# Optimization experiments

Measured on AMD Instinct MI355X. Metric: run time of the kernel, lower is better.

Reference implementation:

```python
import jax, jax.numpy as jnp
import numpy as np


def setup_inputs() -> dict:
    key = jax.random.key(0)
    ks = jax.random.split(key, 6)
    T, B, I, H = 2048, 64, 512, 512
    return {
        "x_seq": jax.random.normal(ks[0], (T, B, I), dtype=jnp.float32),
        "h0": jax.random.normal(ks[1], (B, H), dtype=jnp.float32),
        "Wx_f": jax.random.normal(ks[2], (H, I), dtype=jnp.float32) * (1.0 / np.sqrt(I)),
        "Wh_f": jax.random.normal(ks[3], (H, H), dtype=jnp.float32) * (1.0 / np.sqrt(H)),
        "b_f": jnp.zeros((H,), dtype=jnp.float32),
        "Wx_h": jax.random.normal(ks[4], (H, I), dtype=jnp.float32) * (1.0 / np.sqrt(I)),
        "Wh_h": jax.random.normal(ks[5], (H, H), dtype=jnp.float32) * (1.0 / np.sqrt(H)),
        "b_h": jnp.zeros((H,), dtype=jnp.float32),
    }


def reference(x_seq, h0, Wx_f, Wh_f, b_f, Wx_h, Wh_h, b_h):
    # Precompute the input projections for all timesteps in two big GEMMs
    # (same math as per-step mm(x, Wx.T) + b inside the loop).
    xf = jnp.einsum("tbi,hi->tbh", x_seq, Wx_f) + b_f  # [T,B,H]
    xh = jnp.einsum("tbi,hi->tbh", x_seq, Wx_h) + b_h  # [T,B,H]

    def step(h, xs):
        xf_t, xh_t = xs
        f = jax.nn.sigmoid(xf_t + h @ Wh_f.T)           # forget gate [B,H]
        h_t = jnp.tanh((f * h) @ Wh_h.T + xh_t)          # candidate [B,H]
        h_new = (1.0 - f) * h + f * h_t                  # blend
        return h_new, h_new

    h_final, y_seq = jax.lax.scan(step, h0, (xf, xh))
    return y_seq, h_final
```

## Files before the change

kernel.cpp:

```cpp
#include <hip/hip_runtime.h>
#include <hip/hip_bf16.h>

#define T_STEPS 2048
#define BATCH   64
#define HID     512
#define NBG 2
#define NCG 16
#define CHUNK 32

typedef unsigned short u16;
typedef unsigned int u32;
typedef unsigned long long u64;
typedef __attribute__((ext_vector_type(4))) float f32x4;
typedef __attribute__((ext_vector_type(8))) short bf16x8;

static __device__ __forceinline__ u16 f2bf(float f) {
  union { float f; unsigned u; } v; v.f = f;
  unsigned u = v.u;
  return (u16)((u + 0x7fffu + ((u >> 16) & 1u)) >> 16);
}
static __device__ __forceinline__ float bf2f(u16 h) {
  union { unsigned u; float f; } v; v.u = ((unsigned)h) << 16; return v.f;
}

static __device__ __forceinline__ void st_rlx32(u32* p, u32 v) {
  __hip_atomic_store(p, v, __ATOMIC_RELAXED, __HIP_MEMORY_SCOPE_AGENT);
}
static __device__ __forceinline__ u64 ld_rlx64(const u64* p) {
  return __hip_atomic_load(p, __ATOMIC_RELAXED, __HIP_MEMORY_SCOPE_AGENT);
}
static __device__ __forceinline__ int ld_rlx_i(const int* p) {
  return __hip_atomic_load(p, __ATOMIC_RELAXED, __HIP_MEMORY_SCOPE_AGENT);
}
static __device__ __forceinline__ void st_rlx_i(int* p, int v) {
  __hip_atomic_store(p, v, __ATOMIC_RELAXED, __HIP_MEMORY_SCOPE_AGENT);
}

__global__ __launch_bounds__(256) void cvt_weights(
    const float* __restrict__ wxf, const float* __restrict__ wxh,
    const float* __restrict__ whf, const float* __restrict__ whh,
    u16* __restrict__ o_wxf, u16* __restrict__ o_wxh,
    u16* __restrict__ o_whf, u16* __restrict__ o_whh) {
  int i = blockIdx.x * 256 + threadIdx.x;
  o_wxf[i] = f2bf(wxf[i]);
  o_wxh[i] = f2bf(wxh[i]);
  o_whf[i] = f2bf(whf[i]);
  o_whh[i] = f2bf(whh[i]);
}

__global__ __launch_bounds__(256) void proj_gemm(
    const float* __restrict__ x,
    const u16* __restrict__ wxf, const u16* __restrict__ wxh,
    const float* __restrict__ b_f, const float* __restrict__ b_h,
    u16* __restrict__ xfo, u16* __restrict__ xho) {
  const int bid = blockIdx.x;
  const int mbase = (bid >> 4) * 64;
  const int nbase = (bid & 15) * 64;
  const int tid = threadIdx.x;
  const int lane = tid & 63, wv = tid >> 6;
  const int l15 = lane & 15, lhi = lane >> 4;
  __shared__ u16 a_lds[64 * 48];

  const u16* bptr[4];
#pragma unroll
  for (int ntt = 0; ntt < 4; ++ntt) {
    int n = nbase + ntt * 16 + l15;
    bptr[ntt] = (n < 512) ? (wxf + (size_t)n * 512) : (wxh + (size_t)(n - 512) * 512);
  }
  const int arow = tid >> 2;
  const int akq = (tid & 3) * 8;
  const float* asrc = x + (size_t)(mbase + arow) * 512 + akq;

  f32x4 acc[4];
#pragma unroll
  for (int i = 0; i < 4; ++i) acc[i] = (f32x4){0.f, 0.f, 0.f, 0.f};

  for (int kk = 0; kk < 512; kk += 32) {
    float4 v0 = *(const float4*)(asrc + kk);
    float4 v1 = *(const float4*)(asrc + kk + 4);
    u16* dst = &a_lds[arow * 48 + akq];
    dst[0] = f2bf(v0.x); dst[1] = f2bf(v0.y); dst[2] = f2bf(v0.z); dst[3] = f2bf(v0.w);
    dst[4] = f2bf(v1.x); dst[5] = f2bf(v1.y); dst[6] = f2bf(v1.z); dst[7] = f2bf(v1.w);
    __syncthreads();
    bf16x8 a = *(const bf16x8*)&a_lds[(wv * 16 + l15) * 48 + lhi * 8];
#pragma unroll
    for (int ntt = 0; ntt < 4; ++ntt) {
      bf16x8 b = *(const bf16x8*)(bptr[ntt] + kk + lhi * 8);
      acc[ntt] = __builtin_amdgcn_mfma_f32_16x16x32_bf16(a, b, acc[ntt], 0, 0, 0);
    }
    __syncthreads();
  }
#pragma unroll
  for (int ntt = 0; ntt < 4; ++ntt) {
    int n = nbase + ntt * 16 + l15;
    float bias = (n < 512) ? b_f[n] : b_h[n - 512];
    u16* op = (n < 512) ? (xfo + n) : (xho + (n - 512));
#pragma unroll
    for (int q = 0; q < 4; ++q) {
      int row = mbase + wv * 16 + lhi * 4 + q;
      op[(size_t)row * 512] = f2bf(acc[ntt][q] + bias);
    }
  }
}

__global__ __launch_bounds__(256) void mgu_scan(
    const float* __restrict__ h0,
    const u16* __restrict__ whf, const u16* __restrict__ whh,
    const u16* __restrict__ xf, const u16* __restrict__ xh,
    int* hflags, int* gflags, u16* hexch, u16* gexch,
    float* __restrict__ y, float* __restrict__ hfin) {
  const int bg = blockIdx.x / NCG;
  const int cg = blockIdx.x % NCG;
  const int tid = threadIdx.x;
  const int lane = tid & 63;
  const int wv = tid >> 6;
  const int l15 = lane & 15, lhi = lane >> 4;
  const int mt = wv & 1, nt = wv >> 1;

  __shared__ u16 w_lds[2 * 2 * 16 * 64 * 8];
  __shared__ u16 h_lds[32 * 512];

  for (int s = tid; s < 4096; s += 256) {
    int ln = s & 63;
    int kb = (s >> 6) & 15;
    int wnt = (s >> 10) & 1;
    int which = s >> 11;
    int n = cg * CHUNK + wnt * 16 + (ln & 15);
    int k = kb * 32 + (ln >> 4) * 8;
    const u16* src = (which ? whh : whf) + (size_t)n * 512 + k;
    *(bf16x8*)&w_lds[(((which * 2 + wnt) * 16 + kb) * 64 + ln) * 8] = *(const bf16x8*)src;
  }

  const int rowbase = bg * 32;
  const int r_a = mt * 16 + l15;
  const int cloc = nt * 16 + l15;
  const int gcol = cg * CHUNK + cloc;
  const int myflag = (bg * NCG + cg) * 16;

  for (int t = 0; t < T_STEPS; ++t) {
    if (t == 0) {
      for (int s = tid; s < 2048; s += 256) {
        int r = s >> 6, g8 = s & 63;
        int slot = (g8 + r) & 63;
        const float* src = h0 + (size_t)(rowbase + r) * 512 + g8 * 8;
        u16* dst = &h_lds[r * 512 + slot * 8];
#pragma unroll
        for (int j = 0; j < 8; ++j) dst[j] = f2bf(src[j]);
      }
    } else {
      if (tid < NCG) {
        const int fidx = (bg * NCG + tid) * 16;
        while (ld_rlx_i(&hflags[fidx]) < t) {}
      }
      __syncthreads();
      const u16* src0 = hexch + ((t - 1) & 3) * (BATCH * 512) + rowbase * 512;
      for (int s = tid; s < 2048; s += 256) {
        int r = s >> 6, g8 = s & 63;
        int slot = (g8 + r) & 63;
        const u64* p = (const u64*)(src0 + r * 512 + g8 * 8);
        u64 lo = ld_rlx64(p);
        u64 hi = ld_rlx64(p + 1);
        u64* d = (u64*)&h_lds[r * 512 + slot * 8];
        d[0] = lo; d[1] = hi;
      }
    }
    __syncthreads();

    f32x4 acc = {0.f, 0.f, 0.f, 0.f};
#pragma unroll
    for (int kb = 0; kb < 16; ++kb) {
      int slot = (kb * 4 + lhi + r_a) & 63;
      bf16x8 a = *(const bf16x8*)&h_lds[r_a * 512 + slot * 8];
      bf16x8 b = *(const bf16x8*)&w_lds[((nt * 16 + kb) * 64 + lane) * 8];
      acc = __builtin_amdgcn_mfma_f32_16x16x32_bf16(a, b, acc, 0, 0, 0);
    }

    float fv[4], hv[4];
    const u16* xfp = xf + ((size_t)t * BATCH + rowbase) * 512 + gcol;
#pragma unroll
    for (int q = 0; q < 4; ++q) {
      int r = mt * 16 + lhi * 4 + q;
      float pre = acc[q] + bf2f(xfp[(size_t)r * 512]);
      float f = 1.f / (1.f + __expf(-pre));
      int slot = ((gcol >> 3) + r) & 63;
      float h = bf2f(h_lds[r * 512 + slot * 8 + (gcol & 7)]);
      fv[q] = f; hv[q] = h;
    }
    {
      u32* gx32 = (u32*)(gexch + (t & 3) * (BATCH * 512) + rowbase * 512);
#pragma unroll
      for (int q = 0; q < 4; ++q) {
        float g = fv[q] * hv[q];
        float og = __shfl_xor(g, 1);
        if (!(l15 & 1)) {
          int r = mt * 16 + lhi * 4 + q;
          u32 w = (u32)f2bf(g) | ((u32)f2bf(og) << 16);
          st_rlx32(gx32 + r * 256 + (gcol >> 1), w);
        }
      }
    }
    asm volatile("s_waitcnt vmcnt(0)" ::: "memory");
    __syncthreads();
    if (tid == 0) st_rlx_i(&gflags[myflag], t + 1);

    if (tid < NCG) {
      const int fidx = (bg * NCG + tid) * 16;
      while (ld_rlx_i(&gflags[fidx]) < t + 1) {}
    }
    __syncthreads();
    {
      const u16* src0 = gexch + (t & 3) * (BATCH * 512) + rowbase * 512;
      for (int s = tid; s < 2048; s += 256) {
        int r = s >> 6, g8 = s & 63;
        int slot = (g8 + r) & 63;
        const u64* p = (const u64*)(src0 + r * 512 + g8 * 8);
        u64 lo = ld_rlx64(p);
        u64 hi = ld_rlx64(p + 1);
        u64* d = (u64*)&h_lds[r * 512 + slot * 8];
        d[0] = lo; d[1] = hi;
      }
    }
    __syncthreads();

    f32x4 acc2 = {0.f, 0.f, 0.f, 0.f};
#pragma unroll
    for (int kb = 0; kb < 16; ++kb) {
      int slot = (kb * 4 + lhi + r_a) & 63;
      bf16x8 a = *(const bf16x8*)&h_lds[r_a * 512 + slot * 8];
      bf16x8 b = *(const bf16x8*)&w_lds[(((2 + nt) * 16 + kb) * 64 + lane) * 8];
      acc2 = __builtin_amdgcn_mfma_f32_16x16x32_bf16(a, b, acc2, 0, 0, 0);
    }
    const u16* xhp = xh + ((size_t)t * BATCH + rowbase) * 512 + gcol;
    float* yp = y + ((size_t)t * BATCH + rowbase) * 512 + gcol;
    u32* hx32 = (u32*)(hexch + (t & 3) * (BATCH * 512) + rowbase * 512);
    float hnv[4];
#pragma unroll
    for (int q = 0; q < 4; ++q) {
      int r = mt * 16 + lhi * 4 + q;
      float pre = acc2[q] + bf2f(xhp[(size_t)r * 512]);
      float e = __expf(-2.f * fabsf(pre));
      float ht = copysignf((1.f - e) / (1.f + e), pre);
      float hn = (1.f - fv[q]) * hv[q] + fv[q] * ht;
      hnv[q] = hn;
      yp[(size_t)r * 512] = hn;
      if (t == T_STEPS - 1) hfin[(rowbase + r) * 512 + gcol] = hn;
    }
#pragma unroll
    for (int q = 0; q < 4; ++q) {
      float hn = hnv[q];
      float oh = __shfl_xor(hn, 1);
      if (!(l15 & 1)) {
        int r = mt * 16 + lhi * 4 + q;
        u32 w = (u32)f2bf(hn) | ((u32)f2bf(oh) << 16);
        st_rlx32(hx32 + r * 256 + (gcol >> 1), w);
      }
    }
    asm volatile("s_waitcnt vmcnt(0)" ::: "memory");
    __syncthreads();
    if (tid == 0) st_rlx_i(&hflags[myflag], t + 1);
  }
}

extern "C" void kernel_launch(void* const* d_in, const int* in_sizes, int n_in,
                              void* d_out, int out_size, void* d_ws, size_t ws_size,
                              hipStream_t stream) {
  const float* x   = (const float*)d_in[0];
  const float* h0  = (const float*)d_in[1];
  const float* Wxf = (const float*)d_in[2];
  const float* Whf = (const float*)d_in[3];
  const float* bf_ = (const float*)d_in[4];
  const float* Wxh = (const float*)d_in[5];
  const float* Whh = (const float*)d_in[6];
  const float* bh_ = (const float*)d_in[7];
  float* y = (float*)d_out;
  float* hfin = y + (size_t)T_STEPS * BATCH * HID;

  char* ws = (char*)d_ws;
  u16* wxf_b = (u16*)(ws + 0);
  u16* wxh_b = (u16*)(ws + 524288);
  u16* whf_b = (u16*)(ws + 1048576);
  u16* whh_b = (u16*)(ws + 1572864);
  int* hflags = (int*)(ws + 2097152);
  int* gflags = (int*)(ws + 2099200);
  u16* hexch  = (u16*)(ws + 2101248);
  u16* gexch  = (u16*)(ws + 2363392);
  u16* xfw    = (u16*)(ws + 2625536);
  u16* xhw    = (u16*)(ws + 2625536 + 134217728);

  hipLaunchKernelGGL(cvt_weights, dim3(1024), dim3(256), 0, stream,
                     Wxf, Wxh, Whf, Whh, wxf_b, wxh_b, whf_b, whh_b);
  hipLaunchKernelGGL(proj_gemm, dim3(32768), dim3(256), 0, stream,
                     x, wxf_b, wxh_b, bf_, bh_, xfw, xhw);
  hipLaunchKernelGGL(mgu_scan, dim3(NBG * NCG), dim3(256), 0, stream,
                     h0, whf_b, whh_b, xfw, xhw, hflags, gflags, hexch, gexch, y, hfin);
}
```

Measured before the change: 24.31 ms.

## Replace flag-based inter-block sync with tagged data words in exchange buffers

Drops the separate per-block flags, the vmcnt waits and the barrier-then-flag handshakes. Each 32-bit payload of bf16 pairs is now packed with a 32-bit step tag into a 64-bit relaxed store, and consumers poll the data words directly until every tag reaches the expected step. This removes a full flag round trip per exchange, and the xf/xh loads are hoisted to the top of the step to overlap with the waits. In exchange the exchange traffic doubles and a zeroing kernel is added. The design relies on the 64-bit atomic stores being seen whole, and a barrier after the second GEMM guards reuse of the double buffer.

Result: faster. 19.49 ms (-19.8%).

```diff
diff --git a/kernel.cpp b/kernel.cpp
--- a/kernel.cpp
+++ b/kernel.cpp
@@ -23,17 +23,15 @@
   union { unsigned u; float f; } v; v.u = ((unsigned)h) << 16; return v.f;
 }
 
-static __device__ __forceinline__ void st_rlx32(u32* p, u32 v) {
+static __device__ __forceinline__ void st_rlx64(u64* p, u64 v) {
   __hip_atomic_store(p, v, __ATOMIC_RELAXED, __HIP_MEMORY_SCOPE_AGENT);
 }
 static __device__ __forceinline__ u64 ld_rlx64(const u64* p) {
   return __hip_atomic_load(p, __ATOMIC_RELAXED, __HIP_MEMORY_SCOPE_AGENT);
 }
-static __device__ __forceinline__ int ld_rlx_i(const int* p) {
-  return __hip_atomic_load(p, __ATOMIC_RELAXED, __HIP_MEMORY_SCOPE_AGENT);
-}
-static __device__ __forceinline__ void st_rlx_i(int* p, int v) {
-  __hip_atomic_store(p, v, __ATOMIC_RELAXED, __HIP_MEMORY_SCOPE_AGENT);
+
+__global__ __launch_bounds__(256) void zero_exch(u64* __restrict__ p) {
+  p[(size_t)blockIdx.x * 256 + threadIdx.x] = 0ull;
 }
 
 __global__ __launch_bounds__(256) void cvt_weights(
@@ -103,11 +101,48 @@
   }
 }
 
+template <bool SYNC_BEFORE_LDS>
+static __device__ __forceinline__ void stage_exchange(
+    const u64* __restrict__ src0, u32 tag, int tid, u16* h_lds) {
+  u64 w[32];
+#pragma unroll
+  for (int j = 0; j < 8; ++j) {
+    int s = tid + (j << 8);
+    const u64* p = src0 + ((s >> 6) << 8) + ((s & 63) << 2);
+#pragma unroll
+    for (int k = 0; k < 4; ++k) w[j * 4 + k] = ld_rlx64(p + k);
+  }
+  for (;;) {
+    bool ok = true;
+#pragma unroll
+    for (int j = 0; j < 8; ++j) {
+      int s = tid + (j << 8);
+      const u64* p = src0 + ((s >> 6) << 8) + ((s & 63) << 2);
+#pragma unroll
+      for (int k = 0; k < 4; ++k) {
+        if ((u32)(w[j * 4 + k] >> 32) < tag) { w[j * 4 + k] = ld_rlx64(p + k); ok = false; }
+      }
+    }
+    if (ok) break;
+    __builtin_amdgcn_s_sleep(1);
+  }
+  if (SYNC_BEFORE_LDS) __syncthreads();
+#pragma unroll
+  for (int j = 0; j < 8; ++j) {
+    int s = tid + (j << 8);
+    int r = s >> 6, g8 = s & 63;
+    int slot = (g8 + r) & 63;
+    u32* d = (u32*)&h_lds[r * 512 + slot * 8];
+    d[0] = (u32)w[j * 4 + 0]; d[1] = (u32)w[j * 4 + 1];
+    d[2] = (u32)w[j * 4 + 2]; d[3] = (u32)w[j * 4 + 3];
+  }
+}
+
 __global__ __launch_bounds__(256) void mgu_scan(
     const float* __restrict__ h0,
     const u16* __restrict__ whf, const u16* __restrict__ whh,
     const u16* __restrict__ xf, const u16* __restrict__ xh,
-    int* hflags, int* gflags, u16* hexch, u16* gexch,
+    u64* hexch, u64* gexch,
     float* __restrict__ y, float* __restrict__ hfin) {
   const int bg = blockIdx.x / NCG;
   const int cg = blockIdx.x % NCG;
@@ -135,9 +170,18 @@
   const int r_a = mt * 16 + l15;
   const int cloc = nt * 16 + l15;
   const int gcol = cg * CHUNK + cloc;
-  const int myflag = (bg * NCG + cg) * 16;
 
   for (int t = 0; t < T_STEPS; ++t) {
+    const u16* xfp = xf + ((size_t)t * BATCH + rowbase) * 512 + gcol;
+    const u16* xhp = xh + ((size_t)t * BATCH + rowbase) * 512 + gcol;
+    u16 xfv[4], xhv[4];
+#pragma unroll
+    for (int q = 0; q < 4; ++q) {
+      int r = mt * 16 + lhi * 4 + q;
+      xfv[q] = xfp[(size_t)r * 512];
+      xhv[q] = xhp[(size_t)r * 512];
+    }
+
     if (t == 0) {
       for (int s = tid; s < 2048; s += 256) {
         int r = s >> 6, g8 = s & 63;
@@ -148,21 +192,8 @@
         for (int j = 0; j < 8; ++j) dst[j] = f2bf(src[j]);
       }
     } else {
-      if (tid < NCG) {
-        const int fidx = (bg * NCG + tid) * 16;
-        while (ld_rlx_i(&hflags[fidx]) < t) {}
-      }
-      __syncthreads();
-      const u16* src0 = hexch + ((t - 1) & 3) * (BATCH * 512) + rowbase * 512;
-      for (int s = tid; s < 2048; s += 256) {
-        int r = s >> 6, g8 = s & 63;
-        int slot = (g8 + r) & 63;
-        const u64* p = (const u64*)(src0 + r * 512 + g8 * 8);
-        u64 lo = ld_rlx64(p);
-        u64 hi = ld_rlx64(p + 1);
-        u64* d = (u64*)&h_lds[r * 512 + slot * 8];
-        d[0] = lo; d[1] = hi;
-      }
+      const u64* src0 = hexch + (size_t)((t - 1) & 1) * (BATCH * 256) + (size_t)rowbase * 256;
+      stage_exchange<false>(src0, (u32)t, tid, h_lds);
     }
     __syncthreads();
 
@@ -176,49 +207,33 @@
     }
 
     float fv[4], hv[4];
-    const u16* xfp = xf + ((size_t)t * BATCH + rowbase) * 512 + gcol;
 #pragma unroll
     for (int q = 0; q < 4; ++q) {
       int r = mt * 16 + lhi * 4 + q;
-      float pre = acc[q] + bf2f(xfp[(size_t)r * 512]);
+      float pre = acc[q] + bf2f(xfv[q]);
       float f = 1.f / (1.f + __expf(-pre));
-      int slot = ((gcol >> 3) + r) & 63;
-      float h = bf2f(h_lds[r * 512 + slot * 8 + (gcol & 7)]);
+      int slot2 = ((gcol >> 3) + r) & 63;
+      float h = bf2f(h_lds[r * 512 + slot2 * 8 + (gcol & 7)]);
       fv[q] = f; hv[q] = h;
     }
     {
-      u32* gx32 = (u32*)(gexch + (t & 3) * (BATCH * 512) + rowbase * 512);
+      u64* gx = gexch + (size_t)(t & 1) * (BATCH * 256) + (size_t)rowbase * 256;
+      const u32 tg = (u32)(t + 1);
 #pragma unroll
       for (int q = 0; q < 4; ++q) {
         float g = fv[q] * hv[q];
         float og = __shfl_xor(g, 1);
         if (!(l15 & 1)) {
           int r = mt * 16 + lhi * 4 + q;
-          u32 w = (u32)f2bf(g) | ((u32)f2bf(og) << 16);
-          st_rlx32(gx32 + r * 256 + (gcol >> 1), w);
+          u64 wv_ = (u64)((u32)f2bf(g) | ((u32)f2bf(og) << 16)) | ((u64)tg << 32);
+          st_rlx64(gx + r * 256 + (gcol >> 1), wv_);
         }
       }
     }
-    asm volatile("s_waitcnt vmcnt(0)" ::: "memory");
-    __syncthreads();
-    if (tid == 0) st_rlx_i(&gflags[myflag], t + 1);
-
-    if (tid < NCG) {
-      const int fidx = (bg * NCG + tid) * 16;
-      while (ld_rlx_i(&gflags[fidx]) < t + 1) {}
-    }
-    __syncthreads();
+
     {
-      const u16* src0 = gexch + (t & 3) * (BATCH * 512) + rowbase * 512;
-      for (int s = tid; s < 2048; s += 256) {
-        int r = s >> 6, g8 = s & 63;
-        int slot = (g8 + r) & 63;
-        const u64* p = (const u64*)(src0 + r * 512 + g8 * 8);
-        u64 lo = ld_rlx64(p);
-        u64 hi = ld_rlx64(p + 1);
-        u64* d = (u64*)&h_lds[r * 512 + slot * 8];
-        d[0] = lo; d[1] = hi;
-      }
+      const u64* src0 = gexch + (size_t)(t & 1) * (BATCH * 256) + (size_t)rowbase * 256;
+      stage_exchange<true>(src0, (u32)(t + 1), tid, h_lds);
     }
     __syncthreads();
 
@@ -230,34 +245,43 @@
       bf16x8 b = *(const bf16x8*)&w_lds[(((2 + nt) * 16 + kb) * 64 + lane) * 8];
       acc2 = __builtin_amdgcn_mfma_f32_16x16x32_bf16(a, b, acc2, 0, 0, 0);
     }
-    const u16* xhp = xh + ((size_t)t * BATCH + rowbase) * 512 + gcol;
-    float* yp = y + ((size_t)t * BATCH + rowbase) * 512 + gcol;
-    u32* hx32 = (u32*)(hexch + (t & 3) * (BATCH * 512) + rowbase * 512);
+    __syncthreads();
+
     float hnv[4];
 #pragma unroll
     for (int q = 0; q < 4; ++q) {
-      int r = mt * 16 + lhi * 4 + q;
-      float pre = acc2[q] + bf2f(xhp[(size_t)r * 512]);
+      float pre = acc2[q] + bf2f(xhv[q]);
       float e = __expf(-2.f * fabsf(pre));
       float ht = copysignf((1.f - e) / (1.f + e), pre);
-      float hn = (1.f - fv[q]) * hv[q] + fv[q] * ht;
-      hnv[q] = hn;
-      yp[(size_t)r * 512] = hn;
-      if (t == T_STEPS - 1) hfin[(rowbase + r) * 512 + gcol] = hn;
-    }
-#pragma unroll
-    for (int q = 0; q < 4; ++q) {
-      float hn = hnv[q];
-      float oh = __shfl_xor(hn, 1);
-      if (!(l15 & 1)) {
+      hnv[q] = (1.f - fv[q]) * hv[q] + fv[q] * ht;
+    }
+    {
+      u64* hx = hexch + (size_t)(t & 1) * (BATCH * 256) + (size_t)rowbase * 256;
+      const u32 tg = (u32)(t + 1);
+#pragma unroll
+      for (int q = 0; q < 4; ++q) {
+        float hn = hnv[q];
+        float oh = __shfl_xor(hn, 1);
+        if (!(l15 & 1)) {
+          int r = mt * 16 + lhi * 4 + q;
+          u64 wv_ = (u64)((u32)f2bf(hn) | ((u32)f2bf(oh) << 16)) | ((u64)tg << 32);
+          st_rlx64(hx + r * 256 + (gcol >> 1), wv_);
+        }
+      }
+    }
+    float* yp = y + ((size_t)t * BATCH + rowbase) * 512 + gcol;
+#pragma unroll
+    for (int q = 0; q < 4; ++q) {
+      int r = mt * 16 + lhi * 4 + q;
+      yp[(size_t)r * 512] = hnv[q];
+    }
+    if (t == T_STEPS - 1) {
+#pragma unroll
+      for (int q = 0; q < 4; ++q) {
         int r = mt * 16 + lhi * 4 + q;
-        u32 w = (u32)f2bf(hn) | ((u32)f2bf(oh) << 16);
-        st_rlx32(hx32 + r * 256 + (gcol >> 1), w);
-      }
-    }
-    asm volatile("s_waitcnt vmcnt(0)" ::: "memory");
-    __syncthreads();
-    if (tid == 0) st_rlx_i(&hflags[myflag], t + 1);
+        hfin[(size_t)(rowbase + r) * 512 + gcol] = hnv[q];
+      }
+    }
   }
 }
 
@@ -280,17 +304,17 @@
   u16* wxh_b = (u16*)(ws + 524288);
   u16* whf_b = (u16*)(ws + 1048576);
   u16* whh_b = (u16*)(ws + 1572864);
-  int* hflags = (int*)(ws + 2097152);
-  int* gflags = (int*)(ws + 2099200);
-  u16* hexch  = (u16*)(ws + 2101248);
-  u16* gexch  = (u16*)(ws + 2363392);
-  u16* xfw    = (u16*)(ws + 2625536);
-  u16* xhw    = (u16*)(ws + 2625536 + 134217728);
+  u64* hexch = (u64*)(ws + 2097152);
+  u64* gexch = (u64*)(ws + 2359296);
+  u16* xfw   = (u16*)(ws + 2621440);
+  u16* xhw   = (u16*)(ws + 2621440 + 134217728);
+
+  hipLaunchKernelGGL(zero_exch, dim3(256), dim3(256), 0, stream, hexch);
 
   hipLaunchKernelGGL(cvt_weights, dim3(1024), dim3(256), 0, stream,
                      Wxf, Wxh, Whf, Whh, wxf_b, wxh_b, whf_b, whh_b);
   hipLaunchKernelGGL(proj_gemm, dim3(32768), dim3(256), 0, stream,
                      x, wxf_b, wxh_b, bf_, bh_, xfw, xhw);
   hipLaunchKernelGGL(mgu_scan, dim3(NBG * NCG), dim3(256), 0, stream,
-                     h0, whf_b, whh_b, xfw, xhw, hflags, gflags, hexch, gexch, y, hfin);
-}
+                     h0, whf_b, whh_b, xfw, xhw, hexch, gexch, y, hfin);
+}
```
